# Performance work log

Measured on AMD Instinct MI355X. Metric: run time of the kernel, lower is better.

The kernel has to match this reference:

```python
import jax, jax.numpy as jnp
import numpy as np

B, N, IN_DIM = 16, 256, 768
MEM, HID = 300, 64
NEG = -1e30
SLOPE = 0.01  # LeakyReLU negative slope


def setup_inputs() -> dict:
    key = jax.random.key(0)
    ks = jax.random.split(key, 8)
    # binary adjacency mask, float32 as in the torch module's mask_logits math
    adj = (jax.random.uniform(ks[0], (B, N, N)) < 0.3).astype(jnp.float32)
    feature = jax.random.normal(ks[1], (B, N, IN_DIM), jnp.float32)

    def lin(k, fan_in, shape):
        return (jax.random.normal(k, shape, jnp.float32) / np.sqrt(fan_in)).astype(jnp.float32)

    W0 = lin(ks[2], IN_DIM, (IN_DIM, MEM)); b0 = jnp.zeros((MEM,), jnp.float32)
    W1 = lin(ks[3], MEM, (MEM, MEM));       b1 = jnp.zeros((MEM,), jnp.float32)
    A1 = lin(ks[4], 2 * MEM, (2 * MEM, HID)); ab1 = jnp.zeros((HID,), jnp.float32)
    A2 = lin(ks[5], HID, (HID, 1));           ab2 = jnp.zeros((1,), jnp.float32)
    return dict(adj=adj, feature=feature, W0=W0, b0=b0, W1=W1, b1=b1,
                A1=A1, ab1=ab1, A2=A2, ab2=ab2)


def reference(adj, feature, W0, b0, W1, b1, A1, ab1, A2, ab2):
    Bn, Nn = adj.shape[0], adj.shape[1]
    # additive split of the concat-MLP first layer: A1 @ [h_i; h_j] = Wa@h_i + Wb@h_j
    Wa, Wb = A1[:MEM], A1[MEM:]
    a2 = A2[:, 0]
    x = feature
    for Wl, bl in ((W0, b0), (W1, b1)):  # num_layers = 2
        h = x @ Wl + bl                              # [B, N, MEM]
        si = h @ Wa                                  # [B, N, HID] (source half)
        sj = h @ Wb + ab1                            # [B, N, HID] (target half + bias)
        z = jax.nn.relu(si[:, :, None, :] + sj[:, None, :, :])  # [B, N, N, HID]
        e = jnp.einsum('bijh,h->bij', z, a2) + ab2[0]            # [B, N, N]
        e = jnp.where(e > 0, e, SLOPE * e)           # LeakyReLU(0.01)
        logits = e * adj + (1.0 - adj) * NEG         # mask_logits
        # faithful quirk: softmax over the FLATTENED N*N dimension
        att = jax.nn.softmax(logits.reshape(Bn, -1), axis=1).reshape(Bn, Nn, Nn)
        x = jnp.einsum('bij,bjd->bid', att, h)       # bmm aggregation
        # dropout is identity in eval mode
    return x
```

## Files before the change

kernel.cpp:

```cpp
#include <hip/hip_runtime.h>
#include <hip/hip_bf16.h>

static constexpr int Bc = 16;
static constexpr int Nc = 256;
static constexpr float NEGc = -1e30f;
static constexpr float SLOPEc = 0.01f;

using f32x4 = __attribute__((ext_vector_type(4))) float;
using s16x8 = __attribute__((ext_vector_type(8))) short;

__device__ __forceinline__ void mfma16(f32x4& d, s16x8 a, s16x8 b) {
    asm("v_mfma_f32_16x16x32_bf16 %0, %1, %2, %0" : "+v"(d) : "v"(a), "v"(b));
}

__device__ __forceinline__ float wredMax(float v) {
#pragma unroll
    for (int o = 32; o; o >>= 1) v = fmaxf(v, __shfl_xor(v, o, 64));
    return v;
}
__device__ __forceinline__ float wredSum(float v) {
#pragma unroll
    for (int o = 32; o; o >>= 1) v += __shfl_xor(v, o, 64);
    return v;
}

__device__ __forceinline__ unsigned packhi(unsigned u1, unsigned u0) {
    return __builtin_amdgcn_perm(u1, u0, 0x07060302u);
}

__global__ void __launch_bounds__(256) convert_weights(
    const float* __restrict__ W0, const float* __restrict__ W1,
    const float* __restrict__ A1,
    ushort* __restrict__ W0h, ushort* __restrict__ W0l,
    ushort* __restrict__ W1h, ushort* __restrict__ W1l,
    ushort* __restrict__ A1h, ushort* __restrict__ A1l) {
    int off = blockIdx.x * 256 + threadIdx.x;
    if (off >= 48640) return;
    const float* src; ushort *dh, *dl;
    int ch, c, K, cols; bool isA1 = false;
    if (off < 30720) {
        ch = off / 320; c = off - ch * 320; K = 768; cols = 320;
        src = W0; dh = W0h; dl = W0l;
    } else if (off < 43520) {
        off -= 30720;
        ch = off / 320; c = off - ch * 320; K = 300; cols = 320;
        src = W1; dh = W1h; dl = W1l;
    } else {
        off -= 43520;
        ch = off >> 7; c = off & 127; K = 300; cols = 128;
        src = A1; dh = A1h; dl = A1l; isA1 = true;
    }
    float v[8];
#pragma unroll
    for (int e = 0; e < 8; e++) {
        int k = ch * 8 + e;
        float x = 0.f;
        if (k < K) {
            if (isA1) x = (c < 64) ? src[(size_t)k * 64 + c]
                                   : src[(size_t)(300 + k) * 64 + (c - 64)];
            else if (c < 300) x = src[(size_t)k * 300 + c];
        }
        v[e] = x;
    }
    unsigned hu[4], lu[4];
#pragma unroll
    for (int q = 0; q < 4; q++) {
        unsigned u0 = __float_as_uint(v[q * 2]);
        unsigned u1 = __float_as_uint(v[q * 2 + 1]);
        float r0 = v[q * 2] - __uint_as_float(u0 & 0xFFFF0000u);
        float r1 = v[q * 2 + 1] - __uint_as_float(u1 & 0xFFFF0000u);
        hu[q] = packhi(u1, u0);
        lu[q] = packhi(__float_as_uint(r1), __float_as_uint(r0));
    }
    size_t dst = ((size_t)ch * cols + c) * 8;
    *(uint4*)&dh[dst] = make_uint4(hu[0], hu[1], hu[2], hu[3]);
    *(uint4*)&dl[dst] = make_uint4(lu[0], lu[1], lu[2], lu[3]);
}

template<int BM>
__global__ void __launch_bounds__(256) mfma_gemm(
    const float* __restrict__ A, long long Abstr, int AS, int Kp,
    const ushort* __restrict__ Wh, const ushort* __restrict__ Wl,
    long long Wbstr, int WCOLS,
    const float* __restrict__ bias, int biasN,
    float* __restrict__ out, long long Obstr, int OS, int colmax,
    const float* __restrict__ rmx, const float* __restrict__ rsm,
    ushort* __restrict__ TOh, ushort* __restrict__ TOl) {
    constexpr int TPR = 256 / BM;
    constexpr int NF  = 32 / TPR;
    constexpr int NQ  = NF / 4;
    constexpr int FR  = BM / 32;
    constexpr int FC  = 2;
    constexpr int WROW = BM / 2;

    __shared__ __align__(16) short Ah[BM * 32], Al[BM * 32];
    __shared__ __align__(16) short Bh[2048], Bl[2048];
    __shared__ float sclS[256];
    __shared__ float mb[4], sb[4];

    const int tid = threadIdx.x;
    const int lane = tid & 63, wave = tid >> 6;
    const int wm = wave >> 1, wn = wave & 1;
    const int row0 = blockIdx.y * BM, col0 = blockIdx.x * 64;
    const int bz = blockIdx.z;
    const int m = lane & 15, kch = lane >> 4;

    if (rmx) {
        float mv = rmx[bz * 256 + tid];
        float wmx = wredMax(mv);
        if (!lane) mb[wave] = wmx;
        __syncthreads();
        float M = fmaxf(fmaxf(mb[0], mb[1]), fmaxf(mb[2], mb[3]));
        float ex = expf(mv - M);
        float ws = wredSum(rsm[bz * 256 + tid] * ex);
        if (!lane) sb[wave] = ws;
        __syncthreads();
        float S = sb[0] + sb[1] + sb[2] + sb[3];
        sclS[tid] = ex / S;
    }

    const int arow = tid / TPR;
    const int aoff = (tid % TPR) * NF;
    const int bchunk = tid >> 6, bcol = tid & 63;
    const int bsel = (bchunk * 64 + bcol) * 8;

    const float* Ab = A + (size_t)bz * Abstr + (size_t)(row0 + arow) * AS + aoff;
    const ushort* Whb = Wh + (size_t)bz * Wbstr;
    const ushort* Wlb = Wl + (size_t)bz * Wbstr;

    f32x4 acc[FR][FC];
#pragma unroll
    for (int i = 0; i < FR; i++)
#pragma unroll
        for (int j = 0; j < FC; j++)
#pragma unroll
            for (int e = 0; e < 4; e++) acc[i][j][e] = 0.f;

    float fa[NF];
    s16x8 bhv, blv;
#pragma unroll
    for (int q = 0; q < NQ; q++) *(float4*)&fa[q * 4] = *(const float4*)(Ab + q * 4);
    {
        size_t boff = (size_t)bchunk * WCOLS * 8 + (size_t)(col0 + bcol) * 8;
        bhv = *(const s16x8*)(Whb + boff);
        blv = *(const s16x8*)(Wlb + boff);
    }

    for (int k0 = 0; k0 < Kp; k0 += 32) {
        __syncthreads();
#pragma unroll
        for (int q = 0; q < NQ; q++) {
            unsigned u0 = __float_as_uint(fa[q * 4 + 0]);
            unsigned u1 = __float_as_uint(fa[q * 4 + 1]);
            unsigned u2 = __float_as_uint(fa[q * 4 + 2]);
            unsigned u3 = __float_as_uint(fa[q * 4 + 3]);
            float r0 = fa[q * 4 + 0] - __uint_as_float(u0 & 0xFFFF0000u);
            float r1 = fa[q * 4 + 1] - __uint_as_float(u1 & 0xFFFF0000u);
            float r2 = fa[q * 4 + 2] - __uint_as_float(u2 & 0xFFFF0000u);
            float r3 = fa[q * 4 + 3] - __uint_as_float(u3 & 0xFFFF0000u);
            uint2 th, tl;
            th.x = packhi(u1, u0); th.y = packhi(u3, u2);
            tl.x = packhi(__float_as_uint(r1), __float_as_uint(r0));
            tl.y = packhi(__float_as_uint(r3), __float_as_uint(r2));
            int kq = aoff + q * 4;
            int base = ((kq >> 3) * BM + arow) * 8 + (kq & 7);
            *(uint2*)&Ah[base] = th;
            *(uint2*)&Al[base] = tl;
        }
        *(s16x8*)&Bh[bsel] = bhv;
        *(s16x8*)&Bl[bsel] = blv;
        __syncthreads();
        if (k0 + 32 < Kp) {
#pragma unroll
            for (int q = 0; q < NQ; q++)
                *(float4*)&fa[q * 4] = *(const float4*)(Ab + k0 + 32 + q * 4);
            size_t boff = (size_t)(((k0 + 32) >> 3) + bchunk) * WCOLS * 8
                        + (size_t)(col0 + bcol) * 8;
            bhv = *(const s16x8*)(Whb + boff);
            blv = *(const s16x8*)(Wlb + boff);
        }
        s16x8 Afh[FR], Afl[FR], Bfh[FC], Bfl[FC];
#pragma unroll
        for (int fr = 0; fr < FR; fr++) {
            int off = (kch * BM + wm * WROW + fr * 16 + m) * 8;
            Afh[fr] = *(const s16x8*)&Ah[off];
            Afl[fr] = *(const s16x8*)&Al[off];
        }
#pragma unroll
        for (int fc = 0; fc < FC; fc++) {
            int off = ((kch << 6) + wn * 32 + fc * 16 + m) * 8;
            Bfh[fc] = *(const s16x8*)&Bh[off];
            Bfl[fc] = *(const s16x8*)&Bl[off];
        }
#pragma unroll
        for (int fr = 0; fr < FR; fr++)
#pragma unroll
            for (int fc = 0; fc < FC; fc++) {
                mfma16(acc[fr][fc], Afh[fr], Bfh[fc]);
                mfma16(acc[fr][fc], Afl[fr], Bfh[fc]);
                mfma16(acc[fr][fc], Afh[fr], Bfl[fc]);
            }
    }
    asm volatile("s_nop 7\ns_nop 7\ns_nop 7" ::);
    float* ob = out + (size_t)bz * Obstr;
#pragma unroll
    for (int fr = 0; fr < FR; fr++) {
        int rbase = row0 + wm * WROW + fr * 16 + (kch << 2);
#pragma unroll
        for (int fc = 0; fc < FC; fc++) {
            int col = col0 + wn * 32 + fc * 16 + m;
            float bv = (bias && col < biasN) ? bias[col] : 0.f;
            float vv[4];
#pragma unroll
            for (int e = 0; e < 4; e++) vv[e] = acc[fr][fc][e] + bv;
            if (rmx) {
#pragma unroll
                for (int e = 0; e < 4; e++) vv[e] *= sclS[(rbase + e) & 255];
            }
            if (col < colmax) {
#pragma unroll
                for (int e = 0; e < 4; e++)
                    ob[(size_t)(rbase + e) * OS + col] = vv[e];
            }
            if (TOh) {
                unsigned u0 = __float_as_uint(vv[0]);
                unsigned u1 = __float_as_uint(vv[1]);
                unsigned u2 = __float_as_uint(vv[2]);
                unsigned u3 = __float_as_uint(vv[3]);
                float r0 = vv[0] - __uint_as_float(u0 & 0xFFFF0000u);
                float r1 = vv[1] - __uint_as_float(u1 & 0xFFFF0000u);
                float r2 = vv[2] - __uint_as_float(u2 & 0xFFFF0000u);
                float r3 = vv[3] - __uint_as_float(u3 & 0xFFFF0000u);
                uint2 th, tl;
                th.x = packhi(u1, u0); th.y = packhi(u3, u2);
                tl.x = packhi(__float_as_uint(r1), __float_as_uint(r0));
                tl.y = packhi(__float_as_uint(r3), __float_as_uint(r2));
                int k = rbase & 255, bb = rbase >> 8;
                size_t dst = (size_t)bb * 81920 + ((size_t)(k >> 3) * 320 + col) * 8 + (k & 7);
                *(uint2*)&TOh[dst] = th;
                *(uint2*)&TOl[dst] = tl;
            }
        }
    }
}

__global__ void __launch_bounds__(256) scores_kernel(
    const float* __restrict__ SS,
    const float* __restrict__ adj,
    const float* __restrict__ A2, const float* __restrict__ ab1,
    const float* __restrict__ ab2p,
    float* __restrict__ P, float* __restrict__ rmx, float* __restrict__ rsm) {
    int b = blockIdx.x, ic = blockIdx.y;
    int j = threadIdx.x;
    __shared__ __align__(16) float sis[8][68];
    __shared__ __align__(16) float a2s[64], a1s[64];
    __shared__ __align__(16) float E[8][260];

    if (j < 64) { a2s[j] = A2[j]; a1s[j] = ab1[j]; }
    for (int idx = j; idx < 8 * 64; idx += 256) {
        int r = idx >> 6, h = idx & 63;
        sis[r][h] = SS[((size_t)b * Nc + ic * 8 + r) * 128 + h];
    }
    __syncthreads();

    float4 sv4[16];
    const float4* sjp = (const float4*)(SS + ((size_t)b * Nc + j) * 128 + 64);
#pragma unroll
    for (int q = 0; q < 16; q++) {
        float4 t = sjp[q];
        float4 u = *(const float4*)&a1s[q * 4];
        t.x += u.x; t.y += u.y; t.z += u.z; t.w += u.w;
        sv4[q] = t;
    }
    float acc[8] = {};
    for (int hq = 0; hq < 16; hq++) {
        float4 a2q = *(const float4*)&a2s[hq * 4];
        float4 sjq = sv4[hq];
#pragma unroll
        for (int r = 0; r < 8; r++) {
            float4 siq = *(const float4*)&sis[r][hq * 4];
            acc[r] += a2q.x * fmaxf(siq.x + sjq.x, 0.f)
                    + a2q.y * fmaxf(siq.y + sjq.y, 0.f)
                    + a2q.z * fmaxf(siq.z + sjq.z, 0.f)
                    + a2q.w * fmaxf(siq.w + sjq.w, 0.f);
        }
    }
    float ab2v = ab2p[0];
    const float* adjp = adj + ((size_t)b * Nc + ic * 8) * Nc + j;
#pragma unroll
    for (int r = 0; r < 8; r++) {
        float e = acc[r] + ab2v;
        e = e > 0.f ? e : SLOPEc * e;
        float a = adjp[(size_t)r * Nc];
        E[r][j] = (a != 0.f) ? e : NEGc;
    }
    __syncthreads();
    int wv = j >> 6, lane = j & 63;
#pragma unroll
    for (int rr = 0; rr < 2; rr++) {
        int r = wv * 2 + rr;
        float4 q = *(const float4*)&E[r][lane * 4];
        float m4 = fmaxf(fmaxf(q.x, q.y), fmaxf(q.z, q.w));
        float rm = wredMax(m4);
        float4 p;
        p.x = expf(q.x - rm); p.y = expf(q.y - rm);
        p.z = expf(q.z - rm); p.w = expf(q.w - rm);
        float rs = wredSum(p.x + p.y + p.z + p.w);
        int gi = ic * 8 + r;
        *(float4*)(P + ((size_t)b * Nc + gi) * Nc + lane * 4) = p;
        if (lane == 0) { rmx[b * Nc + gi] = rm; rsm[b * Nc + gi] = rs; }
    }
}

extern "C" void kernel_launch(void* const* d_in, const int* in_sizes, int n_in,
                              void* d_out, int out_size, void* d_ws, size_t ws_size,
                              hipStream_t stream) {
    const float* adj     = (const float*)d_in[0];
    const float* feature = (const float*)d_in[1];
    const float* W0      = (const float*)d_in[2];
    const float* b0      = (const float*)d_in[3];
    const float* W1      = (const float*)d_in[4];
    const float* b1      = (const float*)d_in[5];
    const float* A1      = (const float*)d_in[6];
    const float* ab1     = (const float*)d_in[7];
    const float* A2      = (const float*)d_in[8];
    const float* ab2     = (const float*)d_in[9];

    char* ws = (char*)d_ws;
    float*  h    = (float*)(ws);
    float*  x1   = (float*)(ws + 5242880);
    float*  sisj = (float*)(ws + 10485760);
    float*  P    = (float*)(ws + 12582912);
    float*  rmx  = (float*)(ws + 16777216);
    float*  rsm  = (float*)(ws + 16793600);
    ushort* W0h  = (ushort*)(ws + 16809984);
    ushort* W0l  = (ushort*)(ws + 17301504);
    ushort* W1h  = (ushort*)(ws + 17793024);
    ushort* W1l  = (ushort*)(ws + 17997824);
    ushort* A1h  = (ushort*)(ws + 18202624);
    ushort* A1l  = (ushort*)(ws + 18284544);
    ushort* Hh   = (ushort*)(ws + 18366464);
    ushort* Hl   = (ushort*)(ws + 20987904);
    float* outp  = (float*)d_out;

    convert_weights<<<190, 256, 0, stream>>>(W0, W1, A1, W0h, W0l, W1h, W1l, A1h, A1l);

    for (int L = 0; L < 2; L++) {
        const float* X  = L ? x1 : feature;
        const ushort* Wfh = L ? W1h : W0h;
        const ushort* Wfl = L ? W1l : W0l;
        const float* bf = L ? b1 : b0;
        int Kp = L ? 320 : 768;
        int AS = L ? 320 : 768;

        mfma_gemm<64><<<dim3(5, 64, 1), 256, 0, stream>>>(
            X, 0, AS, Kp, Wfh, Wfl, 0, 320, bf, 300,
            h, 0, 320, 320, nullptr, nullptr, Hh, Hl);
        mfma_gemm<64><<<dim3(2, 64, 1), 256, 0, stream>>>(
            h, 0, 320, 320, A1h, A1l, 0, 128, nullptr, 0,
            sisj, 0, 128, 128, nullptr, nullptr, nullptr, nullptr);
        scores_kernel<<<dim3(16, 32), 256, 0, stream>>>(
            sisj, adj, A2, ab1, ab2, P, rmx, rsm);
        if (L == 0)
            mfma_gemm<64><<<dim3(5, 4, 16), 256, 0, stream>>>(
                P, 65536, 256, 256, Hh, Hl, 81920, 320, nullptr, 0,
                x1, 81920, 320, 320, rmx, rsm, nullptr, nullptr);
        else
            mfma_gemm<64><<<dim3(5, 4, 16), 256, 0, stream>>>(
                P, 65536, 256, 256, Hh, Hl, 81920, 320, nullptr, 0,
                outp, 76800, 300, 300, rmx, rsm, nullptr, nullptr);
    }
}
```

Baseline: 115.7 us.

## Fold A1 projection into layer weights to fuse h and si/sj GEMMs

Precomputes W·Wa and W·Wb (and the matching bias terms, with ab1 folded in) in the weight conversion kernel. Each layer then runs one wider GEMM that produces h and si/sj together, instead of a second GEMM that re-reads h. This removes one launch and the h round trip through global memory per layer, and drops the fp32 h buffer. In exchange, the per-call conversion kernel now does a 300-long dot product per weight element, and si/sj come from reassociated products, which changes rounding.

```diff
diff --git a/kernel.cpp b/kernel.cpp
--- a/kernel.cpp
+++ b/kernel.cpp
@@ -28,72 +28,109 @@
     return __builtin_amdgcn_perm(u1, u0, 0x07060302u);
 }
 
-__global__ void __launch_bounds__(256) convert_weights(
-    const float* __restrict__ W0, const float* __restrict__ W1,
-    const float* __restrict__ A1,
-    ushort* __restrict__ W0h, ushort* __restrict__ W0l,
-    ushort* __restrict__ W1h, ushort* __restrict__ W1l,
-    ushort* __restrict__ A1h, ushort* __restrict__ A1l) {
-    int off = blockIdx.x * 256 + threadIdx.x;
-    if (off >= 48640) return;
-    const float* src; ushort *dh, *dl;
-    int ch, c, K, cols; bool isA1 = false;
-    if (off < 30720) {
-        ch = off / 320; c = off - ch * 320; K = 768; cols = 320;
-        src = W0; dh = W0h; dl = W0l;
-    } else if (off < 43520) {
-        off -= 30720;
-        ch = off / 320; c = off - ch * 320; K = 300; cols = 320;
-        src = W1; dh = W1h; dl = W1l;
+__global__ void __launch_bounds__(256) convert_all(
+    const float* __restrict__ W0, const float* __restrict__ b0,
+    const float* __restrict__ W1, const float* __restrict__ b1,
+    const float* __restrict__ A1, const float* __restrict__ ab1,
+    ushort* __restrict__ F0h, ushort* __restrict__ F0l,
+    ushort* __restrict__ F1h, ushort* __restrict__ F1l,
+    float* __restrict__ bias0, float* __restrict__ bias1) {
+    int idx = blockIdx.x * 256 + threadIdx.x;
+    if (idx >= 79232) return;
+
+    if (idx < 43520) {
+        const float* src; ushort *dh, *dl; int K, ch, c;
+        if (idx < 30720) { src = W0; dh = F0h; dl = F0l; K = 768;
+                           ch = idx / 320; c = idx - ch * 320; }
+        else { int off = idx - 30720; src = W1; dh = F1h; dl = F1l; K = 300;
+               ch = off / 320; c = off - ch * 320; }
+        float v[8];
+#pragma unroll
+        for (int e = 0; e < 8; e++) {
+            int k = ch * 8 + e;
+            v[e] = (k < K && c < 300) ? src[(size_t)k * 300 + c] : 0.f;
+        }
+        unsigned hu[4], lu[4];
+#pragma unroll
+        for (int q = 0; q < 4; q++) {
+            unsigned u0 = __float_as_uint(v[q * 2]);
+            unsigned u1 = __float_as_uint(v[q * 2 + 1]);
+            float r0 = v[q * 2] - __uint_as_float(u0 & 0xFFFF0000u);
+            float r1 = v[q * 2 + 1] - __uint_as_float(u1 & 0xFFFF0000u);
+            hu[q] = packhi(u1, u0);
+            lu[q] = packhi(__float_as_uint(r1), __float_as_uint(r0));
+        }
+        size_t dst = ((size_t)ch * 448 + c) * 8;
+        *(uint4*)&dh[dst] = make_uint4(hu[0], hu[1], hu[2], hu[3]);
+        *(uint4*)&dl[dst] = make_uint4(lu[0], lu[1], lu[2], lu[3]);
+    } else if (idx < 78336) {
+        const float* Wsrc; ushort *dh, *dl; int K, ch, c, eh;
+        if (idx < 68096) {
+            int off = idx - 43520; Wsrc = W0; dh = F0h; dl = F0l; K = 768;
+            ch = off >> 8; int rem = off & 255; c = rem >> 1; eh = rem & 1;
+        } else {
+            int off = idx - 68096; Wsrc = W1; dh = F1h; dl = F1l; K = 300;
+            ch = off >> 8; int rem = off & 255; c = rem >> 1; eh = rem & 1;
+        }
+        const float* Wr[4]; float val[4];
+#pragma unroll
+        for (int i = 0; i < 4; i++) {
+            int k = ch * 8 + eh * 4 + i;
+            int kc = k < K ? k : 0;
+            Wr[i] = Wsrc + (size_t)kc * 300;
+            val[i] = (k < K) ? 1.f : 0.f;
+        }
+        const float* a1c = (c < 64) ? (A1 + c) : (A1 + 300 * 64 + (c - 64));
+        float acc[4] = {};
+        for (int m = 0; m < 300; m++) {
+            float av = a1c[(size_t)m * 64];
+#pragma unroll
+            for (int i = 0; i < 4; i++) acc[i] += Wr[i][m] * av;
+        }
+#pragma unroll
+        for (int i = 0; i < 4; i++) acc[i] *= val[i];
+        unsigned hu[2], lu[2];
+#pragma unroll
+        for (int q = 0; q < 2; q++) {
+            unsigned u0 = __float_as_uint(acc[q * 2]);
+            unsigned u1 = __float_as_uint(acc[q * 2 + 1]);
+            float r0 = acc[q * 2] - __uint_as_float(u0 & 0xFFFF0000u);
+            float r1 = acc[q * 2 + 1] - __uint_as_float(u1 & 0xFFFF0000u);
+            hu[q] = packhi(u1, u0);
+            lu[q] = packhi(__float_as_uint(r1), __float_as_uint(r0));
+        }
+        size_t dst = ((size_t)ch * 448 + 320 + c) * 8 + eh * 4;
+        *(uint2*)&dh[dst] = make_uint2(hu[0], hu[1]);
+        *(uint2*)&dl[dst] = make_uint2(lu[0], lu[1]);
     } else {
-        off -= 43520;
-        ch = off >> 7; c = off & 127; K = 300; cols = 128;
-        src = A1; dh = A1h; dl = A1l; isA1 = true;
-    }
-    float v[8];
-#pragma unroll
-    for (int e = 0; e < 8; e++) {
-        int k = ch * 8 + e;
-        float x = 0.f;
-        if (k < K) {
-            if (isA1) x = (c < 64) ? src[(size_t)k * 64 + c]
-                                   : src[(size_t)(300 + k) * 64 + (c - 64)];
-            else if (c < 300) x = src[(size_t)k * 300 + c];
-        }
-        v[e] = x;
-    }
-    unsigned hu[4], lu[4];
-#pragma unroll
-    for (int q = 0; q < 4; q++) {
-        unsigned u0 = __float_as_uint(v[q * 2]);
-        unsigned u1 = __float_as_uint(v[q * 2 + 1]);
-        float r0 = v[q * 2] - __uint_as_float(u0 & 0xFFFF0000u);
-        float r1 = v[q * 2 + 1] - __uint_as_float(u1 & 0xFFFF0000u);
-        hu[q] = packhi(u1, u0);
-        lu[q] = packhi(__float_as_uint(r1), __float_as_uint(r0));
-    }
-    size_t dst = ((size_t)ch * cols + c) * 8;
-    *(uint4*)&dh[dst] = make_uint4(hu[0], hu[1], hu[2], hu[3]);
-    *(uint4*)&dl[dst] = make_uint4(lu[0], lu[1], lu[2], lu[3]);
-}
-
-template<int BM>
+        int off = idx - 78336;
+        int layer = off / 448, col = off - layer * 448;
+        const float* b = layer ? b1 : b0;
+        float v;
+        if (col < 320) {
+            v = (col < 300) ? b[col] : 0.f;
+        } else {
+            int cc = col - 320;
+            const float* a1c = (cc < 64) ? (A1 + cc) : (A1 + 300 * 64 + (cc - 64));
+            float s = 0.f;
+            for (int m = 0; m < 300; m++) s += b[m] * a1c[(size_t)m * 64];
+            v = s + ((cc >= 64) ? ab1[cc - 64] : 0.f);
+        }
+        (layer ? bias1 : bias0)[col] = v;
+    }
+}
+
 __global__ void __launch_bounds__(256) mfma_gemm(
     const float* __restrict__ A, long long Abstr, int AS, int Kp,
     const ushort* __restrict__ Wh, const ushort* __restrict__ Wl,
     long long Wbstr, int WCOLS,
-    const float* __restrict__ bias, int biasN,
+    const float* __restrict__ bias,
     float* __restrict__ out, long long Obstr, int OS, int colmax,
     const float* __restrict__ rmx, const float* __restrict__ rsm,
-    ushort* __restrict__ TOh, ushort* __restrict__ TOl) {
-    constexpr int TPR = 256 / BM;
-    constexpr int NF  = 32 / TPR;
-    constexpr int NQ  = NF / 4;
-    constexpr int FR  = BM / 32;
-    constexpr int FC  = 2;
-    constexpr int WROW = BM / 2;
-
-    __shared__ __align__(16) short Ah[BM * 32], Al[BM * 32];
+    ushort* __restrict__ TOh, ushort* __restrict__ TOl,
+    float* __restrict__ sisjOut) {
+    constexpr int BM = 64;
+    __shared__ __align__(16) short Ah[2048], Al[2048];
     __shared__ __align__(16) short Bh[2048], Bl[2048];
     __shared__ float sclS[256];
     __shared__ float mb[4], sb[4];
@@ -119,8 +156,8 @@
         sclS[tid] = ex / S;
     }
 
-    const int arow = tid / TPR;
-    const int aoff = (tid % TPR) * NF;
+    const int arow = tid >> 2;
+    const int aoff = (tid & 3) * 8;
     const int bchunk = tid >> 6, bcol = tid & 63;
     const int bsel = (bchunk * 64 + bcol) * 8;
 
@@ -128,18 +165,18 @@
     const ushort* Whb = Wh + (size_t)bz * Wbstr;
     const ushort* Wlb = Wl + (size_t)bz * Wbstr;
 
-    f32x4 acc[FR][FC];
-#pragma unroll
-    for (int i = 0; i < FR; i++)
-#pragma unroll
-        for (int j = 0; j < FC; j++)
+    f32x4 acc[2][2];
+#pragma unroll
+    for (int i = 0; i < 2; i++)
+#pragma unroll
+        for (int j = 0; j < 2; j++)
 #pragma unroll
             for (int e = 0; e < 4; e++) acc[i][j][e] = 0.f;
 
-    float fa[NF];
+    float fa[8];
     s16x8 bhv, blv;
-#pragma unroll
-    for (int q = 0; q < NQ; q++) *(float4*)&fa[q * 4] = *(const float4*)(Ab + q * 4);
+    *(float4*)&fa[0] = *(const float4*)(Ab);
+    *(float4*)&fa[4] = *(const float4*)(Ab + 4);
     {
         size_t boff = (size_t)bchunk * WCOLS * 8 + (size_t)(col0 + bcol) * 8;
         bhv = *(const s16x8*)(Whb + boff);
@@ -149,7 +186,7 @@
     for (int k0 = 0; k0 < Kp; k0 += 32) {
         __syncthreads();
 #pragma unroll
-        for (int q = 0; q < NQ; q++) {
+        for (int q = 0; q < 2; q++) {
             unsigned u0 = __float_as_uint(fa[q * 4 + 0]);
             unsigned u1 = __float_as_uint(fa[q * 4 + 1]);
             unsigned u2 = __float_as_uint(fa[q * 4 + 2]);
@@ -171,45 +208,44 @@
         *(s16x8*)&Bl[bsel] = blv;
         __syncthreads();
         if (k0 + 32 < Kp) {
-#pragma unroll
-            for (int q = 0; q < NQ; q++)
-                *(float4*)&fa[q * 4] = *(const float4*)(Ab + k0 + 32 + q * 4);
+            *(float4*)&fa[0] = *(const float4*)(Ab + k0 + 32);
+            *(float4*)&fa[4] = *(const float4*)(Ab + k0 + 36);
             size_t boff = (size_t)(((k0 + 32) >> 3) + bchunk) * WCOLS * 8
                         + (size_t)(col0 + bcol) * 8;
             bhv = *(const s16x8*)(Whb + boff);
             blv = *(const s16x8*)(Wlb + boff);
         }
-        s16x8 Afh[FR], Afl[FR], Bfh[FC], Bfl[FC];
-#pragma unroll
-        for (int fr = 0; fr < FR; fr++) {
-            int off = (kch * BM + wm * WROW + fr * 16 + m) * 8;
+        s16x8 Afh[2], Afl[2], Bfh[2], Bfl[2];
+#pragma unroll
+        for (int fr = 0; fr < 2; fr++) {
+            int off = (kch * BM + wm * 32 + fr * 16 + m) * 8;
             Afh[fr] = *(const s16x8*)&Ah[off];
             Afl[fr] = *(const s16x8*)&Al[off];
         }
 #pragma unroll
-        for (int fc = 0; fc < FC; fc++) {
+        for (int fc = 0; fc < 2; fc++) {
             int off = ((kch << 6) + wn * 32 + fc * 16 + m) * 8;
             Bfh[fc] = *(const s16x8*)&Bh[off];
             Bfl[fc] = *(const s16x8*)&Bl[off];
         }
 #pragma unroll
-        for (int fr = 0; fr < FR; fr++)
-#pragma unroll
-            for (int fc = 0; fc < FC; fc++) {
+        for (int fr = 0; fr < 2; fr++)
+#pragma unroll
+            for (int fc = 0; fc < 2; fc++) {
                 mfma16(acc[fr][fc], Afh[fr], Bfh[fc]);
                 mfma16(acc[fr][fc], Afl[fr], Bfh[fc]);
                 mfma16(acc[fr][fc], Afh[fr], Bfl[fc]);
             }
     }
     asm volatile("s_nop 7\ns_nop 7\ns_nop 7" ::);
-    float* ob = out + (size_t)bz * Obstr;
-#pragma unroll
-    for (int fr = 0; fr < FR; fr++) {
-        int rbase = row0 + wm * WROW + fr * 16 + (kch << 2);
-#pragma unroll
-        for (int fc = 0; fc < FC; fc++) {
+    float* ob = out ? out + (size_t)bz * Obstr : nullptr;
+#pragma unroll
+    for (int fr = 0; fr < 2; fr++) {
+        int rbase = row0 + wm * 32 + fr * 16 + (kch << 2);
+#pragma unroll
+        for (int fc = 0; fc < 2; fc++) {
             int col = col0 + wn * 32 + fc * 16 + m;
-            float bv = (bias && col < biasN) ? bias[col] : 0.f;
+            float bv = bias ? bias[col] : 0.f;
             float vv[4];
 #pragma unroll
             for (int e = 0; e < 4; e++) vv[e] = acc[fr][fc][e] + bv;
@@ -217,12 +253,11 @@
 #pragma unroll
                 for (int e = 0; e < 4; e++) vv[e] *= sclS[(rbase + e) & 255];
             }
-            if (col < colmax) {
+            if (sisjOut && col >= 320) {
 #pragma unroll
                 for (int e = 0; e < 4; e++)
-                    ob[(size_t)(rbase + e) * OS + col] = vv[e];
-            }
-            if (TOh) {
+                    sisjOut[(size_t)(rbase + e) * 128 + (col - 320)] = vv[e];
+            } else if (TOh) {
                 unsigned u0 = __float_as_uint(vv[0]);
                 unsigned u1 = __float_as_uint(vv[1]);
                 unsigned u2 = __float_as_uint(vv[2]);
@@ -239,6 +274,10 @@
                 size_t dst = (size_t)bb * 81920 + ((size_t)(k >> 3) * 320 + col) * 8 + (k & 7);
                 *(uint2*)&TOh[dst] = th;
                 *(uint2*)&TOl[dst] = tl;
+            } else if (ob && col < colmax) {
+#pragma unroll
+                for (int e = 0; e < 4; e++)
+                    ob[(size_t)(rbase + e) * OS + col] = vv[e];
             }
         }
     }
@@ -247,16 +286,15 @@
 __global__ void __launch_bounds__(256) scores_kernel(
     const float* __restrict__ SS,
     const float* __restrict__ adj,
-    const float* __restrict__ A2, const float* __restrict__ ab1,
-    const float* __restrict__ ab2p,
+    const float* __restrict__ A2, const float* __restrict__ ab2p,
     float* __restrict__ P, float* __restrict__ rmx, float* __restrict__ rsm) {
     int b = blockIdx.x, ic = blockIdx.y;
     int j = threadIdx.x;
     __shared__ __align__(16) float sis[8][68];
-    __shared__ __align__(16) float a2s[64], a1s[64];
+    __shared__ __align__(16) float a2s[64];
     __shared__ __align__(16) float E[8][260];
 
-    if (j < 64) { a2s[j] = A2[j]; a1s[j] = ab1[j]; }
+    if (j < 64) a2s[j] = A2[j];
     for (int idx = j; idx < 8 * 64; idx += 256) {
         int r = idx >> 6, h = idx & 63;
         sis[r][h] = SS[((size_t)b * Nc + ic * 8 + r) * 128 + h];
@@ -266,12 +304,7 @@
     float4 sv4[16];
     const float4* sjp = (const float4*)(SS + ((size_t)b * Nc + j) * 128 + 64);
 #pragma unroll
-    for (int q = 0; q < 16; q++) {
-        float4 t = sjp[q];
-        float4 u = *(const float4*)&a1s[q * 4];
-        t.x += u.x; t.y += u.y; t.z += u.z; t.w += u.w;
-        sv4[q] = t;
-    }
+    for (int q = 0; q < 16; q++) sv4[q] = sjp[q];
     float acc[8] = {};
     for (int hq = 0; hq < 16; hq++) {
         float4 a2q = *(const float4*)&a2s[hq * 4];
@@ -327,47 +360,44 @@
     const float* ab2     = (const float*)d_in[9];
 
     char* ws = (char*)d_ws;
-    float*  h    = (float*)(ws);
-    float*  x1   = (float*)(ws + 5242880);
-    float*  sisj = (float*)(ws + 10485760);
-    float*  P    = (float*)(ws + 12582912);
-    float*  rmx  = (float*)(ws + 16777216);
-    float*  rsm  = (float*)(ws + 16793600);
-    ushort* W0h  = (ushort*)(ws + 16809984);
-    ushort* W0l  = (ushort*)(ws + 17301504);
-    ushort* W1h  = (ushort*)(ws + 17793024);
-    ushort* W1l  = (ushort*)(ws + 17997824);
-    ushort* A1h  = (ushort*)(ws + 18202624);
-    ushort* A1l  = (ushort*)(ws + 18284544);
-    ushort* Hh   = (ushort*)(ws + 18366464);
-    ushort* Hl   = (ushort*)(ws + 20987904);
-    float* outp  = (float*)d_out;
-
-    convert_weights<<<190, 256, 0, stream>>>(W0, W1, A1, W0h, W0l, W1h, W1l, A1h, A1l);
+    float*  x1    = (float*)(ws);
+    float*  sisj  = (float*)(ws + 5242880);
+    float*  P     = (float*)(ws + 7340032);
+    float*  rmx   = (float*)(ws + 11534336);
+    float*  rsm   = (float*)(ws + 11550720);
+    float*  bias0 = (float*)(ws + 11567104);
+    float*  bias1 = (float*)(ws + 11568896);
+    ushort* F0h   = (ushort*)(ws + 11570688);
+    ushort* F0l   = (ushort*)(ws + 12258816);
+    ushort* F1h   = (ushort*)(ws + 12946944);
+    ushort* F1l   = (ushort*)(ws + 13233664);
+    ushort* Hh    = (ushort*)(ws + 13520384);
+    ushort* Hl    = (ushort*)(ws + 16141824);
+    float* outp   = (float*)d_out;
+
+    convert_all<<<310, 256, 0, stream>>>(W0, b0, W1, b1, A1, ab1,
+                                         F0h, F0l, F1h, F1l, bias0, bias1);
 
     for (int L = 0; L < 2; L++) {
-        const float* X  = L ? x1 : feature;
-        const ushort* Wfh = L ? W1h : W0h;
-        const ushort* Wfl = L ? W1l : W0l;
-        const float* bf = L ? b1 : b0;
+        const float* X = L ? x1 : feature;
+        const ushort* Fh = L ? F1h : F0h;
+        const ushort* Fl = L ? F1l : F0l;
+        const float* bf = L ? bias1 : bias0;
         int Kp = L ? 320 : 768;
         int AS = L ? 320 : 768;
 
-        mfma_gemm<64><<<dim3(5, 64, 1), 256, 0, stream>>>(
-            X, 0, AS, Kp, Wfh, Wfl, 0, 320, bf, 300,
-            h, 0, 320, 320, nullptr, nullptr, Hh, Hl);
-        mfma_gemm<64><<<dim3(2, 64, 1), 256, 0, stream>>>(
-            h, 0, 320, 320, A1h, A1l, 0, 128, nullptr, 0,
-            sisj, 0, 128, 128, nullptr, nullptr, nullptr, nullptr);
+        mfma_gemm<<<dim3(7, 64, 1), 256, 0, stream>>>(
+            X, 0, AS, Kp, Fh, Fl, 0, 448, bf,
+            nullptr, 0, 0, 0, nullptr, nullptr, Hh, Hl, sisj);
         scores_kernel<<<dim3(16, 32), 256, 0, stream>>>(
-            sisj, adj, A2, ab1, ab2, P, rmx, rsm);
+            sisj, adj, A2, ab2, P, rmx, rsm);
         if (L == 0)
-            mfma_gemm<64><<<dim3(5, 4, 16), 256, 0, stream>>>(
-                P, 65536, 256, 256, Hh, Hl, 81920, 320, nullptr, 0,
-                x1, 81920, 320, 320, rmx, rsm, nullptr, nullptr);
+            mfma_gemm<<<dim3(5, 4, 16), 256, 0, stream>>>(
+                P, 65536, 256, 256, Hh, Hl, 81920, 320, nullptr,
+                x1, 81920, 320, 320, rmx, rsm, nullptr, nullptr, nullptr);
         else
-            mfma_gemm<64><<<dim3(5, 4, 16), 256, 0, stream>>>(
-                P, 65536, 256, 256, Hh, Hl, 81920, 320, nullptr, 0,
-                outp, 76800, 300, 300, rmx, rsm, nullptr, nullptr);
-    }
-}
+            mfma_gemm<<<dim3(5, 4, 16), 256, 0, stream>>>(
+                P, 65536, 256, 256, Hh, Hl, 81920, 320, nullptr,
+                outp, 76800, 300, 300, rmx, rsm, nullptr, nullptr, nullptr);
+    }
+}
```

Measured after the change: 103.6 us. 1.12x faster.
